# Kernel tuning notes

Measured on AMD Instinct MI355X. Metric: run time of the kernel, lower is better.

Reference implementation:

```python
import jax, jax.numpy as jnp
import numpy as np

NEG_INF = -1e9


def setup_inputs() -> dict:
    key = jax.random.key(0)
    k1, k2, k3 = jax.random.split(key, 3)
    B, C, Q, D = 64, 1024, 128, 128
    context = jax.random.normal(k1, (B, C, D), dtype=jnp.float32)
    query = jax.random.normal(k2, (B, Q, D), dtype=jnp.float32)
    W = jax.random.normal(k3, (3 * D, 1), dtype=jnp.float32)
    query_mask = jnp.ones((B, Q), dtype=jnp.float32)
    return {"context": context, "query": query, "W": W, "query_mask": query_mask}


def reference(context, query, W, query_mask):
    # Dense(1) over concat([c, q, c*q]) decomposes as c.w_c + q.w_q + (c*w_s).q
    D = context.shape[-1]
    w = W[:, 0]
    w_c, w_q, w_s = w[:D], w[D:2 * D], w[2 * D:]
    c_term = jnp.einsum('bcd,d->bc', context, w_c)          # [B,C]
    q_term = jnp.einsum('bqd,d->bq', query, w_q)            # [B,Q]
    s_term = jnp.einsum('bcd,bqd->bcq', context * w_s, query)  # [B,C,Q]
    S = c_term[:, :, None] + q_term[:, None, :] + s_term    # [B,C,Q]
    S = S + (1.0 - query_mask)[:, None, :] * NEG_INF
    c2q_scores = jax.nn.softmax(S, axis=2)                  # [B,C,Q]
    c2q = jnp.einsum('bcq,bqd->bcd', c2q_scores, query)     # [B,C,D]
    q2c_scores = jax.nn.softmax(jnp.max(S, axis=2), axis=1)  # [B,C]
    q2c = jnp.einsum('bc,bcd->bd', q2c_scores, context)     # [B,D]
    q2c = q2c[:, None, :]                                   # broadcast over C
    out = jnp.concatenate([context, c2q, context * c2q, context * q2c], axis=-1)
    return out
```

## Files before the change

kernel.cpp:

```cpp
#include <hip/hip_runtime.h>

#define NEGINF -1000000000.0f

typedef __attribute__((ext_vector_type(4))) float f32x4;
typedef _Float16 half8 __attribute__((ext_vector_type(8)));
typedef _Float16 half4 __attribute__((ext_vector_type(4)));

constexpr int Bn = 64, Cn = 1024, Qn = 128, Dn = 128;
constexpr int QSTR = 136;
constexpr int CSTR = 132;


__global__ __launch_bounds__(512, 4) void k1_kernel(
    const float* __restrict__ ctx, const float* __restrict__ qry,
    const float* __restrict__ W, const float* __restrict__ mask,
    float* __restrict__ out, float* __restrict__ ws_part, float* __restrict__ ws_ms)
{
    __shared__ char smem[72768];
    _Float16* qrow = (_Float16*)smem;
    _Float16* qT2  = (_Float16*)(smem + 34816);
    float* wfull = (float*)(smem + 69632);
    float* qts   = (float*)(smem + 71168);
    float* mloc  = (float*)(smem + 71680);
    float* wv    = (float*)(smem + 72192);
    float* red   = (float*)(smem + 72704);
    float* cq    = (float*)smem;
    float* partf = (float*)(smem + 34816);

    const int b = blockIdx.y, cg = blockIdx.x, c0 = cg * 128;
    const int t = threadIdx.x;
    const float* ctxB = ctx + (size_t)b * Cn * Dn;
    const float* qryB = qry + (size_t)b * Qn * Dn;

    if (t < 384) wfull[t] = W[t];
    __syncthreads();

    {
        int q = t >> 2, h = t & 3;
        const float* qr = qryB + q * Dn + h * 32;
        int p = ((q >> 5) << 5) + 8 * ((q >> 2) & 3) + (q & 3) + 4 * ((q >> 4) & 1);
        float acc = 0.f;
        for (int j = 0; j < 32; j += 4) {
            f32x4 v = *(const f32x4*)(qr + j);
            int d = h * 32 + j;
            acc += v.x * wfull[128 + d] + v.y * wfull[128 + d + 1]
                 + v.z * wfull[128 + d + 2] + v.w * wfull[128 + d + 3];
            half4 hv;
            hv[0] = (_Float16)v.x; hv[1] = (_Float16)v.y;
            hv[2] = (_Float16)v.z; hv[3] = (_Float16)v.w;
            *(half4*)&qrow[q * QSTR + d] = hv;
            qT2[(d + 0) * QSTR + p] = hv[0];
            qT2[(d + 1) * QSTR + p] = hv[1];
            qT2[(d + 2) * QSTR + p] = hv[2];
            qT2[(d + 3) * QSTR + p] = hv[3];
        }
        acc += __shfl_xor(acc, 1);
        acc += __shfl_xor(acc, 2);
        if (h == 0) qts[q] = acc + (1.0f - mask[b * Qn + q]) * NEGINF;
    }
    __syncthreads();

    const int wave = t >> 6, lane = t & 63, g = lane >> 4, l15 = lane & 15;
    const int cw = wave * 16;
    const int cl = cw + l15;

    f32x4 acc1[8] = {};
    float cterm = 0.f;
#pragma unroll
    for (int kk = 0; kk < 4; ++kk) {
        const int dbase = kk * 32 + g * 8;
        const float* pc = ctxB + (size_t)(c0 + cl) * Dn + dbase;
        f32x4 v0 = *(const f32x4*)pc, v1 = *(const f32x4*)(pc + 4);
        f32x4 s0 = *(const f32x4*)&wfull[256 + dbase], s1 = *(const f32x4*)&wfull[256 + dbase + 4];
        f32x4 c0w = *(const f32x4*)&wfull[dbase], c1w = *(const f32x4*)&wfull[dbase + 4];
        cterm += v0.x * c0w.x + v0.y * c0w.y + v0.z * c0w.z + v0.w * c0w.w
               + v1.x * c1w.x + v1.y * c1w.y + v1.z * c1w.z + v1.w * c1w.w;
        half8 ah;
        ah[0] = (_Float16)(v0.x * s0.x); ah[1] = (_Float16)(v0.y * s0.y);
        ah[2] = (_Float16)(v0.z * s0.z); ah[3] = (_Float16)(v0.w * s0.w);
        ah[4] = (_Float16)(v1.x * s1.x); ah[5] = (_Float16)(v1.y * s1.y);
        ah[6] = (_Float16)(v1.z * s1.z); ah[7] = (_Float16)(v1.w * s1.w);
#pragma unroll
        for (int mt = 0; mt < 8; ++mt) {
            half8 qf = *(const half8*)&qrow[(mt * 16 + l15) * QSTR + dbase];
            acc1[mt] = __builtin_amdgcn_mfma_f32_16x16x32_f16(qf, ah, acc1[mt], 0, 0, 0);
        }
    }
    cterm += __shfl_xor(cterm, 16);
    cterm += __shfl_xor(cterm, 32);

#pragma unroll
    for (int mt = 0; mt < 8; ++mt)
#pragma unroll
        for (int r = 0; r < 4; ++r) acc1[mt][r] += qts[mt * 16 + g * 4 + r];

    float mx = -3.4e38f;
#pragma unroll
    for (int mt = 0; mt < 8; ++mt)
#pragma unroll
        for (int r = 0; r < 4; ++r) mx = fmaxf(mx, acc1[mt][r]);
    mx = fmaxf(mx, __shfl_xor(mx, 16));
    mx = fmaxf(mx, __shfl_xor(mx, 32));
    float sum = 0.f;
#pragma unroll
    for (int mt = 0; mt < 8; ++mt)
#pragma unroll
        for (int r = 0; r < 4; ++r) {
            float pv = __expf(acc1[mt][r] - mx);
            acc1[mt][r] = pv;
            sum += pv;
        }
    sum += __shfl_xor(sum, 16);
    sum += __shfl_xor(sum, 32);
    if (g == 0) mloc[cl] = mx + cterm;

    half8 pa[4];
#pragma unroll
    for (int kk2 = 0; kk2 < 4; ++kk2)
#pragma unroll
        for (int j = 0; j < 8; ++j)
            pa[kk2][j] = (_Float16)acc1[2 * kk2 + (j >> 2)][j & 3];

    float inv[4];
#pragma unroll
    for (int r = 0; r < 4; ++r) inv[r] = 1.0f / __shfl(sum, g * 4 + r);

    f32x4 acc2[8] = {};
#pragma unroll
    for (int kk2 = 0; kk2 < 4; ++kk2)
#pragma unroll
        for (int ntD = 0; ntD < 8; ++ntD) {
            half8 qb = *(const half8*)&qT2[(ntD * 16 + l15) * QSTR + kk2 * 32 + 8 * g];
            acc2[ntD] = __builtin_amdgcn_mfma_f32_16x16x32_f16(pa[kk2], qb, acc2[ntD], 0, 0, 0);
        }
    __syncthreads();

#pragma unroll
    for (int r = 0; r < 4; ++r) {
        int c = cw + g * 4 + r;
        float is = inv[r];
#pragma unroll
        for (int ntD = 0; ntD < 8; ++ntD)
            cq[c * CSTR + ntD * 16 + l15] = acc2[ntD][r] * is;
    }
    __syncthreads();

    const int grp = t >> 5, d4 = (t & 31) * 4;
#pragma unroll
    for (int step = 0; step < 8; ++step) {
        int c = grp + step * 16;
        f32x4 q = *(const f32x4*)&cq[c * CSTR + d4];
        f32x4 cv = *(const f32x4*)(ctxB + (size_t)(c0 + c) * Dn + d4);
        float* orow = out + ((size_t)(b * Cn + c0 + c)) * 512;
        *(f32x4*)(orow + d4) = cv;
        *(f32x4*)(orow + 128 + d4) = q;
        f32x4 pr;
        pr.x = cv.x * q.x; pr.y = cv.y * q.y; pr.z = cv.z * q.z; pr.w = cv.w * q.w;
        *(f32x4*)(orow + 256 + d4) = pr;
    }

    float vm = mloc[t & 127];
    float m = vm;
#pragma unroll
    for (int off = 1; off < 64; off <<= 1) m = fmaxf(m, __shfl_xor(m, off));
    if (lane == 0) red[wave] = m;
    __syncthreads();
    float Mloc = red[0];
#pragma unroll
    for (int i = 1; i < 8; ++i) Mloc = fmaxf(Mloc, red[i]);
    float e = __expf(vm - Mloc);
    if (t < 128) wv[t] = e;
    float s = e;
#pragma unroll
    for (int off = 1; off < 64; off <<= 1) s += __shfl_xor(s, off);
    if (lane == 0) red[8 + wave] = s;
    __syncthreads();
    float Sloc = red[8] + red[9];

    {
        const float* cb = ctxB + (size_t)(c0 + grp * 8) * Dn;
        f32x4 a = {};
#pragma unroll
        for (int i = 0; i < 8; ++i) {
            f32x4 cv = *(const f32x4*)(cb + (size_t)i * Dn + d4);
            float w = wv[grp * 8 + i];
            a.x += w * cv.x; a.y += w * cv.y; a.z += w * cv.z; a.w += w * cv.w;
        }
        *(f32x4*)&partf[grp * 128 + d4] = a;
    }
    __syncthreads();
    if (t < 128) {
        float s2 = 0.f;
#pragma unroll
        for (int g2 = 0; g2 < 16; ++g2) s2 += partf[g2 * 128 + t];
        ws_part[((size_t)(b * 8 + cg)) * 128 + t] = s2;
    }
    if (t == 0) {
        ws_ms[(b * 8 + cg) * 2 + 0] = Mloc;
        ws_ms[(b * 8 + cg) * 2 + 1] = Sloc;
    }
}

__global__ __launch_bounds__(256) void k3_kernel(
    const float* __restrict__ ctx, const float* __restrict__ ws_part,
    const float* __restrict__ ws_ms, float* __restrict__ out)
{
    __shared__ float q2cs[128];
    const int ct = blockIdx.x, b = blockIdx.y, t = threadIdx.x;
    if (t < 128) {
        const float* ms = ws_ms + b * 16;
        float Mg = -3.4e38f;
#pragma unroll
        for (int i = 0; i < 8; ++i) Mg = fmaxf(Mg, ms[2 * i]);
        float num = 0.f, den = 0.f;
#pragma unroll
        for (int i = 0; i < 8; ++i) {
            float e = __expf(ms[2 * i] - Mg);
            num += e * ws_part[((size_t)(b * 8 + i)) * 128 + t];
            den += e * ms[2 * i + 1];
        }
        q2cs[t] = num / den;
    }
    __syncthreads();
    const float* cb = ctx + ((size_t)b * Cn + ct * 128) * Dn;
    float* ob = out + ((size_t)(b * Cn) + ct * 128) * 512;
    for (int step = 0; step < 16; ++step) {
        int c = (t >> 5) + step * 8, d4 = (t & 31) * 4;
        f32x4 v = *(const f32x4*)(cb + (size_t)c * Dn + d4);
        f32x4 q = *(const f32x4*)&q2cs[d4];
        f32x4 w;
        w.x = v.x * q.x; w.y = v.y * q.y; w.z = v.z * q.z; w.w = v.w * q.w;
        *(f32x4*)(ob + (size_t)c * 512 + 384 + d4) = w;
    }
}

extern "C" void kernel_launch(void* const* d_in, const int* in_sizes, int n_in,
                              void* d_out, int out_size, void* d_ws, size_t ws_size,
                              hipStream_t stream) {
    const float* ctx  = (const float*)d_in[0];
    const float* qry  = (const float*)d_in[1];
    const float* W    = (const float*)d_in[2];
    const float* mask = (const float*)d_in[3];
    float* out = (float*)d_out;

    float* ws_part = (float*)d_ws;
    float* ws_ms   = ws_part + (size_t)Bn * 8 * 128;

    k1_kernel<<<dim3(8, Bn), 512, 0, stream>>>(ctx, qry, W, mask, out, ws_part, ws_ms);
    k3_kernel<<<dim3(8, Bn), 256, 0, stream>>>(ctx, ws_part, ws_ms, out);
}
```

Before: 49.35 us.

## Precompute fp16 query layouts in a prologue kernel and use nontemporal output stores

Adds a per-batch k0 kernel that converts the query to fp16 once in both row and permuted-transposed layouts and computes the masked q-term. k1 then copies these prepared tiles straight into shared memory, so the query conversion and the scattered transpose are no longer repeated by all 8 context-group blocks of each batch. The copy of the raw context into the output moves from k1 to k3, and output writes now use nontemporal stores. The cost is an extra kernel launch and a workspace round trip for the fp16 query data.

Result: slower. 51.46 us (+4.3%).

```diff
diff --git a/kernel.cpp b/kernel.cpp
--- a/kernel.cpp
+++ b/kernel.cpp
@@ -10,54 +10,88 @@
 constexpr int QSTR = 136;
 constexpr int CSTR = 132;
 
-
-__global__ __launch_bounds__(512, 4) void k1_kernel(
-    const float* __restrict__ ctx, const float* __restrict__ qry,
-    const float* __restrict__ W, const float* __restrict__ mask,
-    float* __restrict__ out, float* __restrict__ ws_part, float* __restrict__ ws_ms)
+__global__ __launch_bounds__(512) void k0_kernel(
+    const float* __restrict__ qry, const float* __restrict__ W,
+    const float* __restrict__ mask,
+    _Float16* __restrict__ qh, _Float16* __restrict__ qT2p, float* __restrict__ qts_g)
 {
-    __shared__ char smem[72768];
-    _Float16* qrow = (_Float16*)smem;
-    _Float16* qT2  = (_Float16*)(smem + 34816);
-    float* wfull = (float*)(smem + 69632);
-    float* qts   = (float*)(smem + 71168);
-    float* mloc  = (float*)(smem + 71680);
-    float* wv    = (float*)(smem + 72192);
-    float* red   = (float*)(smem + 72704);
-    float* cq    = (float*)smem;
-    float* partf = (float*)(smem + 34816);
-
-    const int b = blockIdx.y, cg = blockIdx.x, c0 = cg * 128;
-    const int t = threadIdx.x;
-    const float* ctxB = ctx + (size_t)b * Cn * Dn;
-    const float* qryB = qry + (size_t)b * Qn * Dn;
-
-    if (t < 384) wfull[t] = W[t];
+    __shared__ float wq[128];
+    __shared__ _Float16 qs[128][132];
+    const int b = blockIdx.x, t = threadIdx.x;
+    if (t < 128) wq[t] = W[128 + t];
     __syncthreads();
 
     {
         int q = t >> 2, h = t & 3;
-        const float* qr = qryB + q * Dn + h * 32;
-        int p = ((q >> 5) << 5) + 8 * ((q >> 2) & 3) + (q & 3) + 4 * ((q >> 4) & 1);
+        const float* qr = qry + ((size_t)b * Qn + q) * Dn + h * 32;
         float acc = 0.f;
         for (int j = 0; j < 32; j += 4) {
             f32x4 v = *(const f32x4*)(qr + j);
             int d = h * 32 + j;
-            acc += v.x * wfull[128 + d] + v.y * wfull[128 + d + 1]
-                 + v.z * wfull[128 + d + 2] + v.w * wfull[128 + d + 3];
+            acc += v.x * wq[d] + v.y * wq[d + 1] + v.z * wq[d + 2] + v.w * wq[d + 3];
             half4 hv;
             hv[0] = (_Float16)v.x; hv[1] = (_Float16)v.y;
             hv[2] = (_Float16)v.z; hv[3] = (_Float16)v.w;
-            *(half4*)&qrow[q * QSTR + d] = hv;
-            qT2[(d + 0) * QSTR + p] = hv[0];
-            qT2[(d + 1) * QSTR + p] = hv[1];
-            qT2[(d + 2) * QSTR + p] = hv[2];
-            qT2[(d + 3) * QSTR + p] = hv[3];
+            *(half4*)&qh[((size_t)b * Qn + q) * Dn + d] = hv;
+            *(half4*)&qs[q][d] = hv;
         }
         acc += __shfl_xor(acc, 1);
         acc += __shfl_xor(acc, 2);
-        if (h == 0) qts[q] = acc + (1.0f - mask[b * Qn + q]) * NEGINF;
-    }
+        if (h == 0) qts_g[b * Qn + q] = acc + (1.0f - mask[b * Qn + q]) * NEGINF;
+    }
+    __syncthreads();
+    {
+        int d = t >> 2, h = t & 3;
+#pragma unroll
+        for (int blk = 0; blk < 4; ++blk) {
+            int i0 = h * 32 + blk * 8;
+            half8 w;
+#pragma unroll
+            for (int j = 0; j < 8; ++j) {
+                int i = i0 + j;
+                int q = (i & ~31) | (((i >> 2) & 1) << 4) | (((i >> 3) & 3) << 2) | (i & 3);
+                w[j] = qs[q][d];
+            }
+            *(half8*)&qT2p[((size_t)b * Dn + d) * Qn + i0] = w;
+        }
+    }
+}
+
+__global__ __launch_bounds__(512, 4) void k1_kernel(
+    const float* __restrict__ ctx, const _Float16* __restrict__ qh,
+    const _Float16* __restrict__ qT2p, const float* __restrict__ qts_g,
+    const float* __restrict__ W,
+    float* __restrict__ out, float* __restrict__ ws_part, float* __restrict__ ws_ms)
+{
+    __shared__ char smem[72256];
+    _Float16* qrow = (_Float16*)smem;
+    _Float16* rows = (_Float16*)smem;
+    float* wfull = (float*)(smem + 69632);
+    float* qts   = (float*)(smem + 70656);
+    float* mloc  = (float*)(smem + 71168);
+    float* wv    = (float*)(smem + 71680);
+    float* red   = (float*)(smem + 72192);
+    _Float16* qT2 = (_Float16*)(smem + 34816);
+    float* cq    = (float*)smem;
+    float* partf = (float*)smem;
+
+    const int b = blockIdx.y, cg = blockIdx.x, c0 = cg * 128;
+    const int t = threadIdx.x;
+    const float* ctxB = ctx + (size_t)b * Cn * Dn;
+
+    {
+        int r = t >> 1, h = t & 1;
+        const _Float16* src = (r < 128)
+            ? qh   + ((size_t)b * Qn + r) * Dn + h * 64
+            : qT2p + ((size_t)b * Dn + (r - 128)) * Qn + h * 64;
+        _Float16* dst = rows + r * QSTR + h * 64;
+#pragma unroll
+        for (int s = 0; s < 8; ++s)
+            *(half8*)(dst + s * 8) = *(const half8*)(src + s * 8);
+    }
+    if (t < 128) wfull[t] = W[t];
+    else if (t < 256) wfull[t] = W[256 + (t - 128)];
+    if (t < 128) qts[t] = qts_g[b * Qn + t];
     __syncthreads();
 
     const int wave = t >> 6, lane = t & 63, g = lane >> 4, l15 = lane & 15;
@@ -71,7 +105,7 @@
         const int dbase = kk * 32 + g * 8;
         const float* pc = ctxB + (size_t)(c0 + cl) * Dn + dbase;
         f32x4 v0 = *(const f32x4*)pc, v1 = *(const f32x4*)(pc + 4);
-        f32x4 s0 = *(const f32x4*)&wfull[256 + dbase], s1 = *(const f32x4*)&wfull[256 + dbase + 4];
+        f32x4 s0 = *(const f32x4*)&wfull[128 + dbase], s1 = *(const f32x4*)&wfull[128 + dbase + 4];
         f32x4 c0w = *(const f32x4*)&wfull[dbase], c1w = *(const f32x4*)&wfull[dbase + 4];
         cterm += v0.x * c0w.x + v0.y * c0w.y + v0.z * c0w.z + v0.w * c0w.w
                + v1.x * c1w.x + v1.y * c1w.y + v1.z * c1w.z + v1.w * c1w.w;
@@ -152,11 +186,10 @@
         f32x4 q = *(const f32x4*)&cq[c * CSTR + d4];
         f32x4 cv = *(const f32x4*)(ctxB + (size_t)(c0 + c) * Dn + d4);
         float* orow = out + ((size_t)(b * Cn + c0 + c)) * 512;
-        *(f32x4*)(orow + d4) = cv;
-        *(f32x4*)(orow + 128 + d4) = q;
+        __builtin_nontemporal_store(q, (f32x4*)(orow + 128 + d4));
         f32x4 pr;
         pr.x = cv.x * q.x; pr.y = cv.y * q.y; pr.z = cv.z * q.z; pr.w = cv.w * q.w;
-        *(f32x4*)(orow + 256 + d4) = pr;
+        __builtin_nontemporal_store(pr, (f32x4*)(orow + 256 + d4));
     }
 
     float vm = mloc[t & 127];
@@ -228,9 +261,10 @@
         int c = (t >> 5) + step * 8, d4 = (t & 31) * 4;
         f32x4 v = *(const f32x4*)(cb + (size_t)c * Dn + d4);
         f32x4 q = *(const f32x4*)&q2cs[d4];
+        __builtin_nontemporal_store(v, (f32x4*)(ob + (size_t)c * 512 + d4));
         f32x4 w;
         w.x = v.x * q.x; w.y = v.y * q.y; w.z = v.z * q.z; w.w = v.w * q.w;
-        *(f32x4*)(ob + (size_t)c * 512 + 384 + d4) = w;
+        __builtin_nontemporal_store(w, (f32x4*)(ob + (size_t)c * 512 + 384 + d4));
     }
 }
 
@@ -243,9 +277,13 @@
     const float* mask = (const float*)d_in[3];
     float* out = (float*)d_out;
 
-    float* ws_part = (float*)d_ws;
-    float* ws_ms   = ws_part + (size_t)Bn * 8 * 128;
-
-    k1_kernel<<<dim3(8, Bn), 512, 0, stream>>>(ctx, qry, W, mask, out, ws_part, ws_ms);
+    float* ws_part  = (float*)d_ws;
+    float* ws_ms    = ws_part + (size_t)Bn * 8 * 128;
+    float* qts_g    = ws_ms + (size_t)Bn * 16;
+    _Float16* qh    = (_Float16*)(qts_g + (size_t)Bn * Qn);
+    _Float16* qT2p  = qh + (size_t)Bn * Qn * Dn;
+
+    k0_kernel<<<dim3(Bn), 512, 0, stream>>>(qry, W, mask, qh, qT2p, qts_g);
+    k1_kernel<<<dim3(8, Bn), 512, 0, stream>>>(ctx, qh, qT2p, qts_g, W, out, ws_part, ws_ms);
     k3_kernel<<<dim3(8, Bn), 256, 0, stream>>>(ctx, ws_part, ws_ms, out);
 }
```
